# Performance work log

Hardware: AMD Instinct MI355X
Metric: run time of the kernel (lower is better)

Reference implementation:

```python
import jax, jax.numpy as jnp
import numpy as np

N_NODES = 100000
N_EDGES = 1600000
IN_FEATS = 128
HIDDEN = 150
NUM_OUT = 128


def setup_inputs() -> dict:
    key = jax.random.key(0)
    ks = jax.random.split(key, 9)
    x = jax.random.normal(ks[0], (N_NODES, IN_FEATS), dtype=jnp.float32)
    src = jax.random.randint(ks[1], (N_EDGES,), 0, N_NODES, dtype=jnp.int32)
    dst = jax.random.randint(ks[2], (N_EDGES,), 0, N_NODES, dtype=jnp.int32)
    def lin(k, fan_in, fan_out):
        bound = 1.0 / np.sqrt(fan_in)
        return jax.random.uniform(k, (fan_in, fan_out), jnp.float32, -bound, bound)
    W_self1 = lin(ks[3], IN_FEATS, HIDDEN)
    W_neigh1 = lin(ks[4], IN_FEATS, HIDDEN)
    b1 = jnp.zeros((HIDDEN,), jnp.float32)
    W_self2 = lin(ks[5], HIDDEN, NUM_OUT)
    W_neigh2 = lin(ks[6], HIDDEN, NUM_OUT)
    b2 = jnp.zeros((NUM_OUT,), jnp.float32)
    return {"x": x, "src": src, "dst": dst,
            "W_self1": W_self1, "W_neigh1": W_neigh1, "b1": b1,
            "W_self2": W_self2, "W_neigh2": W_neigh2, "b2": b2}


def _mean_agg(h, src, dst, deg_inv):
    # segment-mean of source features onto destination nodes; isolated nodes -> 0
    summed = jax.ops.segment_sum(h[src], dst, num_segments=N_NODES)
    return summed * deg_inv[:, None]


def _sage_conv(h, src, dst, deg_inv, W_self, W_neigh, b):
    h_neigh = _mean_agg(h, src, dst, deg_inv)
    return h @ W_self + h_neigh @ W_neigh + b


def reference(x, src, dst, W_self1, W_neigh1, b1, W_self2, W_neigh2, b2):
    deg = jax.ops.segment_sum(jnp.ones((src.shape[0],), x.dtype), dst,
                              num_segments=N_NODES)
    deg_inv = jnp.where(deg > 0, 1.0 / jnp.maximum(deg, 1.0), 0.0)
    h = _sage_conv(x, src, dst, deg_inv, W_self1, W_neigh1, b1)
    h = jax.nn.relu(h)
    h = _sage_conv(h, src, dst, deg_inv, W_self2, W_neigh2, b2)
    return h
```

## Files before the change

kernel.cpp:

```cpp
#include <hip/hip_runtime.h>

#define NN 100000
#define NE 1600000
#define INF 128
#define HID 150
#define NOUT 128

#define NBK 196
#define WGS 400
#define EPW 4000
#define CNTL (NBK * WGS)
#define CAP2 10240

typedef __attribute__((ext_vector_type(8))) short bf16x8;
typedef __attribute__((ext_vector_type(8))) unsigned short u16x8;
typedef __attribute__((ext_vector_type(4))) float f32x4;
typedef __attribute__((ext_vector_type(2))) float f32x2;

__device__ inline unsigned short f2bf(float f) {
    unsigned int u = __float_as_uint(f);
    u += 0x7fffu + ((u >> 16) & 1u);
    return (unsigned short)(u >> 16);
}
__device__ inline float bflo(unsigned int t) { return __uint_as_float(t << 16); }
__device__ inline float bfhi(unsigned int t) { return __uint_as_float(t & 0xffff0000u); }


__global__ __launch_bounds__(256) void sort1(const int* __restrict__ src,
                                             const int* __restrict__ dst,
                                             unsigned int* __restrict__ chunkw,
                                             int* __restrict__ cntm) {
    __shared__ int hist[NBK];
    __shared__ int off[NBK];
    __shared__ int s[256];
    __shared__ unsigned int buf[EPW];
    int w = blockIdx.x, tid = threadIdx.x;
    int e0 = w * EPW;
    for (int i = tid; i < NBK; i += 256) hist[i] = 0;
    __syncthreads();
    for (int i = tid; i < EPW; i += 256) atomicAdd(&hist[dst[e0 + i] >> 9], 1);
    __syncthreads();
    int v = (tid < NBK) ? hist[tid] : 0;
    s[tid] = v;
    __syncthreads();
    for (int o = 1; o < 256; o <<= 1) {
        int t = (tid >= o) ? s[tid - o] : 0;
        __syncthreads();
        s[tid] += t;
        __syncthreads();
    }
    if (tid < NBK) {
        off[tid] = s[tid] - v;
        cntm[tid * WGS + w] = v;
    }
    __syncthreads();
    for (int i = tid; i < EPW; i += 256) {
        int d = dst[e0 + i];
        int b = d >> 9;
        int p = atomicAdd(&off[b], 1);
        buf[p] = (unsigned int)src[e0 + i] | ((unsigned int)(d & 511) << 17);
    }
    __syncthreads();
    for (int i = tid; i < EPW; i += 256) chunkw[e0 + i] = buf[i];
}

__global__ void scanA(const int* __restrict__ in, int* __restrict__ excl,
                      int* __restrict__ blk_sums, int L) {
    __shared__ int s[256];
    int i = blockIdx.x * 256 + threadIdx.x;
    int d = (i < L) ? in[i] : 0;
    s[threadIdx.x] = d;
    __syncthreads();
    for (int o = 1; o < 256; o <<= 1) {
        int t = (threadIdx.x >= o) ? s[threadIdx.x - o] : 0;
        __syncthreads();
        s[threadIdx.x] += t;
        __syncthreads();
    }
    int incl = s[threadIdx.x];
    if (i < L) excl[i] = incl - d;
    if (threadIdx.x == 255) blk_sums[blockIdx.x] = incl;
}

__global__ void scanB(int* __restrict__ blk_sums, int nb) {
    __shared__ int s[512];
    int t = threadIdx.x;
    int v = (t < nb) ? blk_sums[t] : 0;
    s[t] = v;
    __syncthreads();
    for (int o = 1; o < 512; o <<= 1) {
        int u = (t >= o) ? s[t - o] : 0;
        __syncthreads();
        s[t] += u;
        __syncthreads();
    }
    if (t < nb) blk_sums[t] = s[t] - v;
}

__global__ void scanC(int* __restrict__ excl, const int* __restrict__ blk_sums, int L) {
    int i = blockIdx.x * 256 + threadIdx.x;
    if (i < L) excl[i] += blk_sums[blockIdx.x];
}

__global__ __launch_bounds__(256) void sort3(const unsigned int* __restrict__ chunkw,
                                             const int* __restrict__ cntm,
                                             const int* __restrict__ offm,
                                             unsigned int* __restrict__ bmaj) {
    __shared__ int excl[NBK + 1];
    __shared__ int dbase[NBK];
    __shared__ int s[256];
    int w = blockIdx.x, tid = threadIdx.x;
    int v = (tid < NBK) ? cntm[tid * WGS + w] : 0;
    if (tid < NBK) dbase[tid] = offm[tid * WGS + w];
    s[tid] = v;
    __syncthreads();
    for (int o = 1; o < 256; o <<= 1) {
        int t = (tid >= o) ? s[tid - o] : 0;
        __syncthreads();
        s[tid] += t;
        __syncthreads();
    }
    if (tid < NBK) excl[tid] = s[tid] - v;
    if (tid == 0) excl[NBK] = EPW;
    __syncthreads();
    int e0 = w * EPW;
    for (int i = tid; i < EPW; i += 256) {
        int lo = 0, hi = NBK;
        while (hi - lo > 1) {
            int mid = (lo + hi) >> 1;
            if (excl[mid] <= i) lo = mid; else hi = mid;
        }
        bmaj[dbase[lo] + (i - excl[lo])] = chunkw[e0 + i];
    }
}

__global__ __launch_bounds__(256) void buildcsr(const unsigned int* __restrict__ bmaj,
                                                const int* __restrict__ offm,
                                                int* __restrict__ csr_ptr,
                                                float* __restrict__ deg_inv,
                                                int* __restrict__ csr_src) {
    __shared__ int cnt[512];
    __shared__ int excl[512];
    __shared__ int off[512];
    __shared__ int s[256];
    __shared__ int span[CAP2];
    int b = blockIdx.x, tid = threadIdx.x;
    int base = offm[b * WGS];
    int nxt = (b == NBK - 1) ? NE : offm[(b + 1) * WGS];
    int n = nxt - base;
    if (n > CAP2) n = CAP2;
    for (int i = tid; i < 512; i += 256) cnt[i] = 0;
    __syncthreads();
    for (int i = tid; i < n; i += 256) atomicAdd(&cnt[bmaj[base + i] >> 17], 1);
    __syncthreads();
    int a0 = cnt[2 * tid], a1 = cnt[2 * tid + 1];
    int ps = a0 + a1;
    s[tid] = ps;
    __syncthreads();
    for (int o = 1; o < 256; o <<= 1) {
        int t = (tid >= o) ? s[tid - o] : 0;
        __syncthreads();
        s[tid] += t;
        __syncthreads();
    }
    int ex = s[tid] - ps;
    excl[2 * tid] = ex;
    excl[2 * tid + 1] = ex + a0;
    off[2 * tid] = ex;
    off[2 * tid + 1] = ex + a0;
    __syncthreads();
    for (int l = tid; l < 512; l += 256) {
        int g = b * 512 + l;
        if (g < NN) {
            csr_ptr[g] = base + excl[l];
            int d = cnt[l];
            deg_inv[g] = d > 0 ? 1.0f / (float)d : 0.0f;
        }
    }
    if (b == NBK - 1 && tid == 0) csr_ptr[NN] = NE;
    for (int i = tid; i < n; i += 256) {
        unsigned int wd = bmaj[base + i];
        int l = wd >> 17;
        int p = atomicAdd(&off[l], 1);
        span[p] = (int)(wd & 0x1FFFFu);
    }
    __syncthreads();
    for (int i = tid; i < n; i += 256) csr_src[base + i] = span[i];
}


__global__ void cast_bf16(const float* __restrict__ in, unsigned short* __restrict__ outb,
                          int n8) {
    int i = blockIdx.x * 256 + threadIdx.x;
    if (i >= n8) return;
    const f32x4* p = (const f32x4*)in;
    f32x4 v0 = __builtin_nontemporal_load(&p[(size_t)i * 2]);
    f32x4 v1 = __builtin_nontemporal_load(&p[(size_t)i * 2 + 1]);
    u16x8 o = {f2bf(v0[0]), f2bf(v0[1]), f2bf(v0[2]), f2bf(v0[3]),
               f2bf(v1[0]), f2bf(v1[1]), f2bf(v1[2]), f2bf(v1[3])};
    ((u16x8*)outb)[i] = o;
}

__global__ void pack_weights(const float* __restrict__ Ws1, const float* __restrict__ Wn1,
                             const float* __restrict__ b1,
                             const float* __restrict__ Ws2, const float* __restrict__ Wn2,
                             unsigned short* __restrict__ W1t, unsigned short* __restrict__ W2t,
                             float* __restrict__ b1p) {
    int id = blockIdx.x * 256 + threadIdx.x;
    if (id < 160 * 256) {
        int n = id >> 8, k = id & 255;
        float v = 0.f;
        if (n < HID) v = (k < 128) ? Ws1[k * HID + n] : Wn1[(k - 128) * HID + n];
        W1t[id] = f2bf(v);
    } else if (id < 160 * 256 + 256 * 160) {
        int id2 = id - 160 * 256;
        int n = id2 / 160, k = id2 - n * 160;
        float v = 0.f;
        if (k < HID) v = (n < 128) ? Ws2[k * 128 + n] : Wn2[k * 128 + (n - 128)];
        W2t[id2] = f2bf(v);
    } else if (id < 160 * 256 + 256 * 160 + 160) {
        int n = id - (160 * 256 + 256 * 160);
        b1p[n] = (n < HID) ? b1[n] : 0.f;
    }
}


#define AGG_ACC(t)                              \
    accA += (f32x2){bflo(t.x), bfhi(t.x)};      \
    accB += (f32x2){bflo(t.y), bfhi(t.y)};      \
    accC += (f32x2){bflo(t.z), bfhi(t.z)};      \
    accD += (f32x2){bflo(t.w), bfhi(t.w)};

#define AGG_BODY(FTBL)                                                 \
    int e = start;                                                     \
    for (; e + 16 <= end; e += 16) {                                   \
        int s0 = csr_src[e + rg];                                      \
        int s1 = csr_src[e + 4 + rg];                                  \
        int s2 = csr_src[e + 8 + rg];                                  \
        int s3 = csr_src[e + 12 + rg];                                 \
        uint4 t0 = FTBL[(size_t)s0 * 16 + ch];                         \
        uint4 t1 = FTBL[(size_t)s1 * 16 + ch];                         \
        uint4 t2 = FTBL[(size_t)s2 * 16 + ch];                         \
        uint4 t3 = FTBL[(size_t)s3 * 16 + ch];                         \
        AGG_ACC(t0);                                                   \
        AGG_ACC(t1);                                                   \
        AGG_ACC(t2);                                                   \
        AGG_ACC(t3);                                                   \
    }                                                                  \
    if (e + 8 <= end) {                                                \
        int s0 = csr_src[e + rg];                                      \
        int s1 = csr_src[e + 4 + rg];                                  \
        uint4 t0 = FTBL[(size_t)s0 * 16 + ch];                         \
        uint4 t1 = FTBL[(size_t)s1 * 16 + ch];                         \
        AGG_ACC(t0);                                                   \
        AGG_ACC(t1);                                                   \
        e += 8;                                                        \
    }                                                                  \
    if (e + 4 <= end) {                                                \
        int s0 = csr_src[e + rg];                                      \
        uint4 t0 = FTBL[(size_t)s0 * 16 + ch];                         \
        AGG_ACC(t0);                                                   \
        e += 4;                                                        \
    }                                                                  \
    int rem = end - e;                                                 \
    if (rem > 0) {                                                     \
        int s0 = csr_src[(rg < rem) ? (e + rg) : e];                   \
        uint4 t = FTBL[(size_t)s0 * 16 + ch];                          \
        float wt = (rg < rem) ? 1.f : 0.f;                             \
        f32x2 w2 = {wt, wt};                                           \
        accA += w2 * (f32x2){bflo(t.x), bfhi(t.x)};                    \
        accB += w2 * (f32x2){bflo(t.y), bfhi(t.y)};                    \
        accC += w2 * (f32x2){bflo(t.z), bfhi(t.z)};                    \
        accD += w2 * (f32x2){bflo(t.w), bfhi(t.w)};                    \
    }                                                                  \
    float acc0 = accA[0], acc1 = accA[1];                              \
    float acc2 = accB[0], acc3 = accB[1];                              \
    float acc4 = accC[0], acc5 = accC[1];                              \
    float acc6 = accD[0], acc7 = accD[1];                              \
    acc0 += __shfl_xor(acc0, 32); acc1 += __shfl_xor(acc1, 32);        \
    acc2 += __shfl_xor(acc2, 32); acc3 += __shfl_xor(acc3, 32);        \
    acc4 += __shfl_xor(acc4, 32); acc5 += __shfl_xor(acc5, 32);        \
    acc6 += __shfl_xor(acc6, 32); acc7 += __shfl_xor(acc7, 32);        \
    acc0 += __shfl_xor(acc0, 16); acc1 += __shfl_xor(acc1, 16);        \
    acc2 += __shfl_xor(acc2, 16); acc3 += __shfl_xor(acc3, 16);        \
    acc4 += __shfl_xor(acc4, 16); acc5 += __shfl_xor(acc5, 16);        \
    acc6 += __shfl_xor(acc6, 16); acc7 += __shfl_xor(acc7, 16);

__global__ __launch_bounds__(256) void agg_mean_q(
    const unsigned short* __restrict__ featb, const int* __restrict__ csr_ptr,
    const float* __restrict__ deg_inv, const int* __restrict__ csr_src,
    unsigned short* __restrict__ outb) {
    int wid = threadIdx.x >> 6;
    int lane = threadIdx.x & 63;
    int v = blockIdx.x * 4 + wid;
    int start = csr_ptr[v], end = csr_ptr[v + 1];
    int rg = lane >> 4, ch = lane & 15;
    const uint4* f4 = (const uint4*)featb;
    f32x2 accA = {0.f, 0.f}, accB = {0.f, 0.f};
    f32x2 accC = {0.f, 0.f}, accD = {0.f, 0.f};
    AGG_BODY(f4);
    if (lane < 16) {
        float di = deg_inv[v];
        u16x8 o = {f2bf(acc0 * di), f2bf(acc1 * di), f2bf(acc2 * di), f2bf(acc3 * di),
                   f2bf(acc4 * di), f2bf(acc5 * di), f2bf(acc6 * di), f2bf(acc7 * di)};
        ((u16x8*)outb)[(size_t)v * 16 + ch] = o;
    }
}

__global__ __launch_bounds__(256) void agg_add_q(
    const unsigned short* __restrict__ zb, const int* __restrict__ csr_ptr,
    const float* __restrict__ deg_inv, const int* __restrict__ csr_src,
    float* __restrict__ out) {
    int wid = threadIdx.x >> 6;
    int lane = threadIdx.x & 63;
    int v = blockIdx.x * 4 + wid;
    int start = csr_ptr[v], end = csr_ptr[v + 1];
    int rg = lane >> 4, ch = lane & 15;
    const uint4* f4 = (const uint4*)zb;
    f32x2 accA = {0.f, 0.f}, accB = {0.f, 0.f};
    f32x2 accC = {0.f, 0.f}, accD = {0.f, 0.f};
    AGG_BODY(f4);
    if (lane < 16) {
        float di = deg_inv[v];
        f32x4* o4 = (f32x4*)out;
        size_t base = (size_t)v * 32 + ch * 2;
        f32x4 c0 = __builtin_nontemporal_load(&o4[base]);
        f32x4 c1 = __builtin_nontemporal_load(&o4[base + 1]);
        c0[0] += acc0 * di; c0[1] += acc1 * di; c0[2] += acc2 * di; c0[3] += acc3 * di;
        c1[0] += acc4 * di; c1[1] += acc5 * di; c1[2] += acc6 * di; c1[3] += acc7 * di;
        __builtin_nontemporal_store(c0, &o4[base]);
        __builtin_nontemporal_store(c1, &o4[base + 1]);
    }
}


__global__ __launch_bounds__(256, 3) void gemm1_mfma(
    const unsigned short* __restrict__ xb, const unsigned short* __restrict__ aggb,
    const unsigned short* __restrict__ W1t, const float* __restrict__ b1p,
    unsigned short* __restrict__ h1b) {
    __shared__ __align__(16) unsigned short A_lds[128][40];
    __shared__ __align__(16) unsigned short B_lds[160][40];
    int tid = threadIdx.x;
    int m0 = blockIdx.x * 128;
    int w = tid >> 6, lane = tid & 63;
    int lrow = lane & 15, quad = lane >> 4;
    int wr = (w & 1) * 64;
    int wc = (w >> 1) * 80;
    f32x4 acc[4][5];
    #pragma unroll
    for (int r = 0; r < 4; r++)
        #pragma unroll
        for (int c = 0; c < 5; c++) acc[r][c] = (f32x4){0.f, 0.f, 0.f, 0.f};

    for (int k0 = 0; k0 < 256; k0 += 32) {
        __syncthreads();
        #pragma unroll
        for (int i = 0; i < 2; i++) {
            int idx = tid + i * 256;
            int row = idx >> 2, ch = idx & 3;
            int gm = m0 + row, gk = k0 + ch * 8;
            u16x8 val = {0, 0, 0, 0, 0, 0, 0, 0};
            if (gm < NN) {
                const unsigned short* sp = (gk < 128)
                    ? (xb + (size_t)gm * 128 + gk)
                    : (aggb + (size_t)gm * 128 + (gk - 128));
                val = *(const u16x8*)sp;
            }
            *(u16x8*)&A_lds[row][ch * 8] = val;
        }
        #pragma unroll
        for (int i = 0; i < 3; i++) {
            int idx = tid + i * 256;
            if (idx < 640) {
                int n = idx >> 2, ch = idx & 3;
                u16x8 val = *(const u16x8*)(W1t + (size_t)n * 256 + k0 + ch * 8);
                *(u16x8*)&B_lds[n][ch * 8] = val;
            }
        }
        __syncthreads();
        bf16x8 a[4], b[5];
        #pragma unroll
        for (int r = 0; r < 4; r++)
            a[r] = *(const bf16x8*)&A_lds[wr + r * 16 + lrow][quad * 8];
        #pragma unroll
        for (int c = 0; c < 5; c++)
            b[c] = *(const bf16x8*)&B_lds[wc + c * 16 + lrow][quad * 8];
        #pragma unroll
        for (int r = 0; r < 4; r++)
            #pragma unroll
            for (int c = 0; c < 5; c++)
                acc[r][c] = __builtin_amdgcn_mfma_f32_16x16x32_bf16(a[r], b[c], acc[r][c], 0, 0, 0);
    }
    #pragma unroll
    for (int r = 0; r < 4; r++) {
        #pragma unroll
        for (int rr = 0; rr < 4; rr++) {
            int gm = m0 + wr + r * 16 + quad * 4 + rr;
            if (gm < NN) {
                #pragma unroll
                for (int c = 0; c < 5; c++) {
                    int gn = wc + c * 16 + lrow;
                    float val = acc[r][c][rr] + b1p[gn];
                    val = val > 0.f ? val : 0.f;
                    h1b[(size_t)gm * 160 + gn] = f2bf(val);
                }
            }
        }
    }
}

__global__ __launch_bounds__(256, 4) void gemm2_mfma(
    const unsigned short* __restrict__ h1b, const unsigned short* __restrict__ W2t,
    const float* __restrict__ b2, float* __restrict__ out,
    unsigned short* __restrict__ zb) {
    __shared__ __align__(16) unsigned short A_lds[128][40];
    __shared__ __align__(16) unsigned short B_lds[128][40];
    int tid = threadIdx.x;
    int m0 = blockIdx.x * 128;
    int n0 = blockIdx.y * 128;
    int w = tid >> 6, lane = tid & 63;
    int lrow = lane & 15, quad = lane >> 4;
    int wr = (w & 1) * 64;
    int wc = (w >> 1) * 64;
    f32x4 acc[4][4];
    #pragma unroll
    for (int r = 0; r < 4; r++)
        #pragma unroll
        for (int c = 0; c < 4; c++) acc[r][c] = (f32x4){0.f, 0.f, 0.f, 0.f};

    for (int k0 = 0; k0 < 160; k0 += 32) {
        __syncthreads();
        #pragma unroll
        for (int i = 0; i < 2; i++) {
            int idx = tid + i * 256;
            int row = idx >> 2, ch = idx & 3;
            int gm = m0 + row;
            u16x8 val = {0, 0, 0, 0, 0, 0, 0, 0};
            if (gm < NN) val = *(const u16x8*)(h1b + (size_t)gm * 160 + k0 + ch * 8);
            *(u16x8*)&A_lds[row][ch * 8] = val;
        }
        #pragma unroll
        for (int i = 0; i < 2; i++) {
            int idx = tid + i * 256;
            int n = idx >> 2, ch = idx & 3;
            u16x8 val = *(const u16x8*)(W2t + (size_t)(n0 + n) * 160 + k0 + ch * 8);
            *(u16x8*)&B_lds[n][ch * 8] = val;
        }
        __syncthreads();
        bf16x8 a[4], b[4];
        #pragma unroll
        for (int r = 0; r < 4; r++)
            a[r] = *(const bf16x8*)&A_lds[wr + r * 16 + lrow][quad * 8];
        #pragma unroll
        for (int c = 0; c < 4; c++)
            b[c] = *(const bf16x8*)&B_lds[wc + c * 16 + lrow][quad * 8];
        #pragma unroll
        for (int r = 0; r < 4; r++)
            #pragma unroll
            for (int c = 0; c < 4; c++)
                acc[r][c] = __builtin_amdgcn_mfma_f32_16x16x32_bf16(a[r], b[c], acc[r][c], 0, 0, 0);
    }
    #pragma unroll
    for (int r = 0; r < 4; r++) {
        #pragma unroll
        for (int rr = 0; rr < 4; rr++) {
            int gm = m0 + wr + r * 16 + quad * 4 + rr;
            if (gm < NN) {
                #pragma unroll
                for (int c = 0; c < 4; c++) {
                    int gn = wc + c * 16 + lrow;
                    float val = acc[r][c][rr];
                    if (n0 == 0) {
                        out[(size_t)gm * 128 + gn] = val + b2[gn];
                    } else {
                        zb[(size_t)gm * 128 + gn] = f2bf(val);
                    }
                }
            }
        }
    }
}


extern "C" void kernel_launch(void* const* d_in, const int* in_sizes, int n_in,
                              void* d_out, int out_size, void* d_ws, size_t ws_size,
                              hipStream_t stream) {
    const float* x   = (const float*)d_in[0];
    const int* src   = (const int*)d_in[1];
    const int* dst   = (const int*)d_in[2];
    const float* Ws1 = (const float*)d_in[3];
    const float* Wn1 = (const float*)d_in[4];
    const float* b1  = (const float*)d_in[5];
    const float* Ws2 = (const float*)d_in[6];
    const float* Wn2 = (const float*)d_in[7];
    const float* b2  = (const float*)d_in[8];
    float* out = (float*)d_out;

    char* p = (char*)d_ws;
    auto carve = [&](size_t bytes) {
        void* r = (void*)p;
        p += (bytes + 255) & ~(size_t)255;
        return r;
    };
    int*   csr_ptr  = (int*)carve((size_t)(NN + 1) * 4);
    float* deg_inv  = (float*)carve((size_t)NN * 4);
    int*   csr_src  = (int*)carve((size_t)NE * 4);
    int*   cntm     = (int*)carve((size_t)CNTL * 4);
    int*   offm     = (int*)carve((size_t)CNTL * 4);
    int*   blk2     = (int*)carve(512 * 4);
    unsigned short* xb   = (unsigned short*)carve((size_t)NN * 128 * 2);
    unsigned short* aggb = (unsigned short*)carve((size_t)NN * 128 * 2);
    unsigned short* zb   = (unsigned short*)carve((size_t)NN * 128 * 2);
    unsigned short* W1t  = (unsigned short*)carve(160 * 256 * 2);
    unsigned short* W2t  = (unsigned short*)carve(256 * 160 * 2);
    float* b1p           = (float*)carve(160 * 4);
    unsigned short* h1b  = (unsigned short*)carve((size_t)NN * 160 * 2);
    unsigned int* chunkw = (unsigned int*)h1b;
    unsigned int* bmaj   = (unsigned int*)((char*)h1b + (size_t)NE * 4);

    sort1<<<WGS, 256, 0, stream>>>(src, dst, chunkw, cntm);
    const int SB = (CNTL + 255) / 256;
    scanA<<<SB, 256, 0, stream>>>(cntm, offm, blk2, CNTL);
    scanB<<<1, 512, 0, stream>>>(blk2, SB);
    scanC<<<SB, 256, 0, stream>>>(offm, blk2, CNTL);
    sort3<<<WGS, 256, 0, stream>>>(chunkw, cntm, offm, bmaj);
    buildcsr<<<NBK, 256, 0, stream>>>(bmaj, offm, csr_ptr, deg_inv, csr_src);

    cast_bf16<<<(NN * 128 / 8 + 255) / 256, 256, 0, stream>>>(x, xb, NN * 128 / 8);
    pack_weights<<<(160 * 256 + 256 * 160 + 160 + 255) / 256, 256, 0, stream>>>(
        Ws1, Wn1, b1, Ws2, Wn2, W1t, W2t, b1p);

    agg_mean_q<<<NN / 4, 256, 0, stream>>>(xb, csr_ptr, deg_inv, csr_src, aggb);
    gemm1_mfma<<<dim3((NN + 127) / 128, 1), 256, 0, stream>>>(xb, aggb, W1t, b1p, h1b);

    gemm2_mfma<<<dim3((NN + 127) / 128, 2), 256, 0, stream>>>(h1b, W2t, b2, out, zb);
    agg_add_q<<<NN / 4, 256, 0, stream>>>(zb, csr_ptr, deg_inv, csr_src, out);

    (void)in_sizes; (void)n_in; (void)out_size; (void)ws_size;
}
```

Baseline: 376.3 us.

## Replace two-pass bucket sort CSR build with atomic degree count and fill

Replaces the bucketed counting-sort CSR construction (sort1/scan/sort3/buildcsr) with a global-atomic degree histogram, a prefix scan over per-node degrees, and an atomic-cursor scatter fill of csr_src. This removes several passes and intermediate buffers but relies on 1.6M global atomics on random addresses twice. The neighbor order within each node becomes nondeterministic, so the bf16 summation order in aggregation is no longer fixed, and the scattered writes have poor locality.

```diff
diff --git a/kernel.cpp b/kernel.cpp
--- a/kernel.cpp
+++ b/kernel.cpp
@@ -6,12 +6,6 @@
 #define HID 150
 #define NOUT 128
 
-#define NBK 196
-#define WGS 400
-#define EPW 4000
-#define CNTL (NBK * WGS)
-#define CAP2 10240
-
 typedef __attribute__((ext_vector_type(8))) short bf16x8;
 typedef __attribute__((ext_vector_type(8))) unsigned short u16x8;
 typedef __attribute__((ext_vector_type(4))) float f32x4;
@@ -26,42 +20,14 @@
 __device__ inline float bfhi(unsigned int t) { return __uint_as_float(t & 0xffff0000u); }
 
 
-__global__ __launch_bounds__(256) void sort1(const int* __restrict__ src,
-                                             const int* __restrict__ dst,
-                                             unsigned int* __restrict__ chunkw,
-                                             int* __restrict__ cntm) {
-    __shared__ int hist[NBK];
-    __shared__ int off[NBK];
-    __shared__ int s[256];
-    __shared__ unsigned int buf[EPW];
-    int w = blockIdx.x, tid = threadIdx.x;
-    int e0 = w * EPW;
-    for (int i = tid; i < NBK; i += 256) hist[i] = 0;
-    __syncthreads();
-    for (int i = tid; i < EPW; i += 256) atomicAdd(&hist[dst[e0 + i] >> 9], 1);
-    __syncthreads();
-    int v = (tid < NBK) ? hist[tid] : 0;
-    s[tid] = v;
-    __syncthreads();
-    for (int o = 1; o < 256; o <<= 1) {
-        int t = (tid >= o) ? s[tid - o] : 0;
-        __syncthreads();
-        s[tid] += t;
-        __syncthreads();
-    }
-    if (tid < NBK) {
-        off[tid] = s[tid] - v;
-        cntm[tid * WGS + w] = v;
-    }
-    __syncthreads();
-    for (int i = tid; i < EPW; i += 256) {
-        int d = dst[e0 + i];
-        int b = d >> 9;
-        int p = atomicAdd(&off[b], 1);
-        buf[p] = (unsigned int)src[e0 + i] | ((unsigned int)(d & 511) << 17);
-    }
-    __syncthreads();
-    for (int i = tid; i < EPW; i += 256) chunkw[e0 + i] = buf[i];
+__global__ void count_deg(const int* __restrict__ dst, int* __restrict__ deg, int n4) {
+    int i = blockIdx.x * 256 + threadIdx.x;
+    if (i >= n4) return;
+    int4 d = ((const int4*)dst)[i];
+    atomicAdd(&deg[d.x], 1);
+    atomicAdd(&deg[d.y], 1);
+    atomicAdd(&deg[d.z], 1);
+    atomicAdd(&deg[d.w], 1);
 }
 
 __global__ void scanA(const int* __restrict__ in, int* __restrict__ excl,
@@ -97,95 +63,30 @@
     if (t < nb) blk_sums[t] = s[t] - v;
 }
 
-__global__ void scanC(int* __restrict__ excl, const int* __restrict__ blk_sums, int L) {
+__global__ void scanC2(int* __restrict__ csr_ptr, const int* __restrict__ blk,
+                       const int* __restrict__ deg, float* __restrict__ deg_inv,
+                       int* __restrict__ cur, int L) {
     int i = blockIdx.x * 256 + threadIdx.x;
-    if (i < L) excl[i] += blk_sums[blockIdx.x];
-}
-
-__global__ __launch_bounds__(256) void sort3(const unsigned int* __restrict__ chunkw,
-                                             const int* __restrict__ cntm,
-                                             const int* __restrict__ offm,
-                                             unsigned int* __restrict__ bmaj) {
-    __shared__ int excl[NBK + 1];
-    __shared__ int dbase[NBK];
-    __shared__ int s[256];
-    int w = blockIdx.x, tid = threadIdx.x;
-    int v = (tid < NBK) ? cntm[tid * WGS + w] : 0;
-    if (tid < NBK) dbase[tid] = offm[tid * WGS + w];
-    s[tid] = v;
-    __syncthreads();
-    for (int o = 1; o < 256; o <<= 1) {
-        int t = (tid >= o) ? s[tid - o] : 0;
-        __syncthreads();
-        s[tid] += t;
-        __syncthreads();
-    }
-    if (tid < NBK) excl[tid] = s[tid] - v;
-    if (tid == 0) excl[NBK] = EPW;
-    __syncthreads();
-    int e0 = w * EPW;
-    for (int i = tid; i < EPW; i += 256) {
-        int lo = 0, hi = NBK;
-        while (hi - lo > 1) {
-            int mid = (lo + hi) >> 1;
-            if (excl[mid] <= i) lo = mid; else hi = mid;
-        }
-        bmaj[dbase[lo] + (i - excl[lo])] = chunkw[e0 + i];
-    }
-}
-
-__global__ __launch_bounds__(256) void buildcsr(const unsigned int* __restrict__ bmaj,
-                                                const int* __restrict__ offm,
-                                                int* __restrict__ csr_ptr,
-                                                float* __restrict__ deg_inv,
-                                                int* __restrict__ csr_src) {
-    __shared__ int cnt[512];
-    __shared__ int excl[512];
-    __shared__ int off[512];
-    __shared__ int s[256];
-    __shared__ int span[CAP2];
-    int b = blockIdx.x, tid = threadIdx.x;
-    int base = offm[b * WGS];
-    int nxt = (b == NBK - 1) ? NE : offm[(b + 1) * WGS];
-    int n = nxt - base;
-    if (n > CAP2) n = CAP2;
-    for (int i = tid; i < 512; i += 256) cnt[i] = 0;
-    __syncthreads();
-    for (int i = tid; i < n; i += 256) atomicAdd(&cnt[bmaj[base + i] >> 17], 1);
-    __syncthreads();
-    int a0 = cnt[2 * tid], a1 = cnt[2 * tid + 1];
-    int ps = a0 + a1;
-    s[tid] = ps;
-    __syncthreads();
-    for (int o = 1; o < 256; o <<= 1) {
-        int t = (tid >= o) ? s[tid - o] : 0;
-        __syncthreads();
-        s[tid] += t;
-        __syncthreads();
-    }
-    int ex = s[tid] - ps;
-    excl[2 * tid] = ex;
-    excl[2 * tid + 1] = ex + a0;
-    off[2 * tid] = ex;
-    off[2 * tid + 1] = ex + a0;
-    __syncthreads();
-    for (int l = tid; l < 512; l += 256) {
-        int g = b * 512 + l;
-        if (g < NN) {
-            csr_ptr[g] = base + excl[l];
-            int d = cnt[l];
-            deg_inv[g] = d > 0 ? 1.0f / (float)d : 0.0f;
-        }
-    }
-    if (b == NBK - 1 && tid == 0) csr_ptr[NN] = NE;
-    for (int i = tid; i < n; i += 256) {
-        unsigned int wd = bmaj[base + i];
-        int l = wd >> 17;
-        int p = atomicAdd(&off[l], 1);
-        span[p] = (int)(wd & 0x1FFFFu);
-    }
-    __syncthreads();
-    for (int i = tid; i < n; i += 256) csr_src[base + i] = span[i];
+    if (i < L) {
+        int v = csr_ptr[i] + blk[blockIdx.x];
+        csr_ptr[i] = v;
+        cur[i] = v;
+        int d = deg[i];
+        deg_inv[i] = d > 0 ? 1.0f / (float)d : 0.0f;
+    }
+    if (i == 0) csr_ptr[L] = NE;
+}
+
+__global__ void fill_csr(const int* __restrict__ src, const int* __restrict__ dst,
+                         int* __restrict__ cur, int* __restrict__ csr_src, int n4) {
+    int i = blockIdx.x * 256 + threadIdx.x;
+    if (i >= n4) return;
+    int4 s = ((const int4*)src)[i];
+    int4 d = ((const int4*)dst)[i];
+    csr_src[atomicAdd(&cur[d.x], 1)] = s.x;
+    csr_src[atomicAdd(&cur[d.y], 1)] = s.y;
+    csr_src[atomicAdd(&cur[d.z], 1)] = s.z;
+    csr_src[atomicAdd(&cur[d.w], 1)] = s.w;
 }
 
 
@@ -505,8 +406,8 @@
     int*   csr_ptr  = (int*)carve((size_t)(NN + 1) * 4);
     float* deg_inv  = (float*)carve((size_t)NN * 4);
     int*   csr_src  = (int*)carve((size_t)NE * 4);
-    int*   cntm     = (int*)carve((size_t)CNTL * 4);
-    int*   offm     = (int*)carve((size_t)CNTL * 4);
+    int*   deg_cnt  = (int*)carve((size_t)NN * 4);
+    int*   cur      = (int*)carve((size_t)NN * 4);
     int*   blk2     = (int*)carve(512 * 4);
     unsigned short* xb   = (unsigned short*)carve((size_t)NN * 128 * 2);
     unsigned short* aggb = (unsigned short*)carve((size_t)NN * 128 * 2);
@@ -515,16 +416,16 @@
     unsigned short* W2t  = (unsigned short*)carve(256 * 160 * 2);
     float* b1p           = (float*)carve(160 * 4);
     unsigned short* h1b  = (unsigned short*)carve((size_t)NN * 160 * 2);
-    unsigned int* chunkw = (unsigned int*)h1b;
-    unsigned int* bmaj   = (unsigned int*)((char*)h1b + (size_t)NE * 4);
-
-    sort1<<<WGS, 256, 0, stream>>>(src, dst, chunkw, cntm);
-    const int SB = (CNTL + 255) / 256;
-    scanA<<<SB, 256, 0, stream>>>(cntm, offm, blk2, CNTL);
-    scanB<<<1, 512, 0, stream>>>(blk2, SB);
-    scanC<<<SB, 256, 0, stream>>>(offm, blk2, CNTL);
-    sort3<<<WGS, 256, 0, stream>>>(chunkw, cntm, offm, bmaj);
-    buildcsr<<<NBK, 256, 0, stream>>>(bmaj, offm, csr_ptr, deg_inv, csr_src);
+
+    hipMemsetAsync(deg_cnt, 0, (size_t)NN * 4, stream);
+    const int N4 = NE / 4;
+    const int EB = (N4 + 255) / 256;
+    count_deg<<<EB, 256, 0, stream>>>(dst, deg_cnt, N4);
+    const int SB2 = (NN + 255) / 256;
+    scanA<<<SB2, 256, 0, stream>>>(deg_cnt, csr_ptr, blk2, NN);
+    scanB<<<1, 512, 0, stream>>>(blk2, SB2);
+    scanC2<<<SB2, 256, 0, stream>>>(csr_ptr, blk2, deg_cnt, deg_inv, cur, NN);
+    fill_csr<<<EB, 256, 0, stream>>>(src, dst, cur, csr_src, N4);
 
     cast_bf16<<<(NN * 128 / 8 + 255) / 256, 256, 0, stream>>>(x, xb, NN * 128 / 8);
     pack_weights<<<(160 * 256 + 256 * 160 + 160 + 255) / 256, 256, 0, stream>>>(
```

Measured after the change: 510.8 us. +35.7%, slower.
